# Kernel optimization log

Hardware: AMD Instinct MI355X
Metric: run time of the kernel (lower is better)

Reference implementation:

```python
import jax, jax.numpy as jnp
import numpy as np

EPS = 1e-6


def rms_norm(h, w):
    # T5-style: no mean subtraction, no bias; variance in fp32
    var = jnp.mean(jnp.square(h.astype(jnp.float32)), axis=-1, keepdims=True)
    h = h * jax.lax.rsqrt(var + EPS)
    return w * h


def split_heads(t, n_heads):
    b, n, d = t.shape
    return t.reshape(b, n, n_heads, d // n_heads).transpose(0, 2, 1, 3)  # [B,H,N,dk]


def unify_heads(t):
    b, h, n, dk = t.shape
    return t.transpose(0, 2, 1, 3).reshape(b, n, h * dk)


def attention(q_in, kv_in, bias, wq, wk, wv, wo, n_heads):
    q = split_heads(q_in @ wq, n_heads)   # [B,H,Nq,dk]
    k = split_heads(kv_in @ wk, n_heads)  # [B,H,Nk,dk]
    v = split_heads(kv_in @ wv, n_heads)
    scores = jnp.einsum('bhqd,bhkd->bhqk', q, k) + bias  # no 1/sqrt(dk) scaling (T5 style)
    w = jax.nn.softmax(scores.astype(jnp.float32), axis=-1).astype(scores.dtype)
    out = jnp.einsum('bhqk,bhkd->bhqd', w, v)
    return unify_heads(out) @ wo


def setup_inputs() -> dict:
    key = jax.random.key(0)
    ks = jax.random.split(key, 18)
    B, N, ENC_N, D, H, DFF = 4, 2048, 1024, 1024, 16, 4096
    s = 0.02
    inp = {
        'x': jax.random.normal(ks[0], (B, N, D), jnp.float32),
        'encoding': jax.random.normal(ks[1], (B, ENC_N, D), jnp.float32),
        'self_attention_position_bias': jax.random.normal(ks[2], (1, H, 1, N), jnp.float32),
        'enc_dec_attention_position_bias': jax.random.normal(ks[3], (1, H, N, ENC_N), jnp.float32),
        'wq_s': jax.random.normal(ks[4], (D, D), jnp.float32) * s,
        'wk_s': jax.random.normal(ks[5], (D, D), jnp.float32) * s,
        'wv_s': jax.random.normal(ks[6], (D, D), jnp.float32) * s,
        'wo_s': jax.random.normal(ks[7], (D, D), jnp.float32) * s,
        'wq_c': jax.random.normal(ks[8], (D, D), jnp.float32) * s,
        'wk_c': jax.random.normal(ks[9], (D, D), jnp.float32) * s,
        'wv_c': jax.random.normal(ks[10], (D, D), jnp.float32) * s,
        'wo_c': jax.random.normal(ks[11], (D, D), jnp.float32) * s,
        'ff1_w': jax.random.normal(ks[12], (D, DFF), jnp.float32) * s,
        'ff2_w': jax.random.normal(ks[13], (DFF, D), jnp.float32) * s,
        'norm1_w': jnp.ones((D,), jnp.float32),
        'norm2_w': jnp.ones((D,), jnp.float32),
        'norm3_w': jnp.ones((D,), jnp.float32),
    }
    return inp


def reference(x, encoding, self_attention_position_bias, enc_dec_attention_position_bias,
              wq_s, wk_s, wv_s, wo_s, wq_c, wk_c, wv_c, wo_c,
              ff1_w, ff2_w, norm1_w, norm2_w, norm3_w):
    n_heads = 16
    # --- self-attention (decoder: single query = last token) ---
    normed = rms_norm(x, norm1_w)
    q_in = normed[:, -1:, :]  # [B,1,D]
    attn_out = attention(q_in, normed, self_attention_position_bias,
                         wq_s, wk_s, wv_s, wo_s, n_heads)  # [B,1,D]
    x = x + attn_out  # broadcast over sequence, matching torch in-place broadcast
    # --- cross-attention ---
    normed = rms_norm(x, norm2_w)
    cross_out = attention(normed, encoding, enc_dec_attention_position_bias,
                          wq_c, wk_c, wv_c, wo_c, n_heads)  # [B,N,D]
    x = x + cross_out
    # --- MLP ---
    normed = rms_norm(x, norm3_w)
    mlp_out = jax.nn.relu(normed @ ff1_w) @ ff2_w
    return x + mlp_out
```

## Files before the change

kernel.cpp:

```cpp
#include <hip/hip_runtime.h>
#include <stdint.h>

typedef unsigned short bfu;
typedef __bf16 bf8v __attribute__((ext_vector_type(8)));
typedef unsigned short us8 __attribute__((ext_vector_type(8)));
typedef unsigned short us4 __attribute__((ext_vector_type(4)));
typedef float f4v __attribute__((ext_vector_type(4)));

__device__ __forceinline__ float bf2f(bfu u) {
    union { unsigned u; float f; } c; c.u = ((unsigned)u) << 16; return c.f;
}
__device__ __forceinline__ bfu f2bf(float f) {
    union { float f; unsigned u; } c; c.f = f;
    unsigned r = c.u + 0x7fffu + ((c.u >> 16) & 1u);
    return (bfu)(r >> 16);
}
__device__ __forceinline__ f4v mfma16(us8 a, us8 b, f4v c) {
    return __builtin_amdgcn_mfma_f32_16x16x32_bf16(
        __builtin_bit_cast(bf8v, a), __builtin_bit_cast(bf8v, b), c, 0, 0, 0);
}

template<int BM, int BN, int EPI>
__global__ __launch_bounds__(256) void gemm_bt(
    const bfu* __restrict__ A, const bfu* __restrict__ Bt,
    const float* __restrict__ resF, void* __restrict__ outP,
    int K, int lda, int ldb, int ldc)
{
    constexpr int BK = 64;
    constexpr int WM = BM / 2, WN = BN / 2;
    constexpr int TM = WM / 16, TN = WN / 16;
    __shared__ __align__(16) bfu sA[BM * BK];
    __shared__ __align__(16) bfu sB[BN * BK];

    const int tid  = threadIdx.x;
    const int lane = tid & 63;
    const int wid  = tid >> 6;
    const int wr = wid >> 1, wc = wid & 1;

    const int m0 = blockIdx.y * BM;
    const int n0 = blockIdx.x * BN;

    f4v acc[TM][TN];
    #pragma unroll
    for (int i = 0; i < TM; ++i)
        #pragma unroll
        for (int j = 0; j < TN; ++j)
            acc[i][j] = (f4v)0.0f;

    const bfu* gA = A + (long long)m0 * lda;
    const bfu* gB = Bt + (long long)n0 * ldb;
    const int rsub = tid >> 3;
    const int kb   = (tid & 7) * 8;

    for (int k0 = 0; k0 < K; k0 += BK) {
        us8 ra[BM / 32], rb[BN / 32];
        #pragma unroll
        for (int it = 0; it < BM / 32; ++it)
            ra[it] = *(const us8*)(gA + (long long)(it * 32 + rsub) * lda + k0 + kb);
        #pragma unroll
        for (int it = 0; it < BN / 32; ++it)
            rb[it] = *(const us8*)(gB + (long long)(it * 32 + rsub) * ldb + k0 + kb);

        __syncthreads();
        #pragma unroll
        for (int it = 0; it < BM / 32; ++it)
            *(us8*)&sA[(it * 32 + rsub) * BK + kb] = ra[it];
        #pragma unroll
        for (int it = 0; it < BN / 32; ++it)
            *(us8*)&sB[(it * 32 + rsub) * BK + kb] = rb[it];
        __syncthreads();

        #pragma unroll
        for (int kk = 0; kk < BK; kk += 32) {
            const int kro = kk + ((lane >> 4) << 3);
            us8 af[TM], bfr[TN];
            #pragma unroll
            for (int i = 0; i < TM; ++i)
                af[i] = *(const us8*)&sA[(wr * WM + i * 16 + (lane & 15)) * BK + kro];
            #pragma unroll
            for (int j = 0; j < TN; ++j)
                bfr[j] = *(const us8*)&sB[(wc * WN + j * 16 + (lane & 15)) * BK + kro];
            #pragma unroll
            for (int i = 0; i < TM; ++i)
                #pragma unroll
                for (int j = 0; j < TN; ++j)
                    acc[i][j] = mfma16(af[i], bfr[j], acc[i][j]);
        }
    }

    const int quad = lane >> 4;
    const int cn = lane & 15;
    #pragma unroll
    for (int i = 0; i < TM; ++i) {
        #pragma unroll
        for (int j = 0; j < TN; ++j) {
            const int col = n0 + wc * WN + j * 16 + cn;
            #pragma unroll
            for (int r = 0; r < 4; ++r) {
                const int row = m0 + wr * WM + i * 16 + quad * 4 + r;
                const long long idx = (long long)row * ldc + col;
                const float v = acc[i][j][r];
                if constexpr (EPI == 0) ((bfu*)outP)[idx] = f2bf(v);
                else if constexpr (EPI == 1) ((float*)outP)[idx] = resF[idx] + v;
                else ((bfu*)outP)[idx] = f2bf(fmaxf(v, 0.0f));
            }
        }
    }
}

#define SROW 1036
__global__ __launch_bounds__(256, 4) void xattn(
    const bfu* __restrict__ q2,
    const bfu* __restrict__ kv2,
    const bfu* __restrict__ v2t,
    const float* __restrict__ bias,
    bfu* __restrict__ O)
{
    __shared__ __align__(16) bfu S[16 * SROW];
    const int tid = threadIdx.x, lane = tid & 63, wid = tid >> 6;
    const int quad = lane >> 4, l16 = lane & 15;
    const int bh = blockIdx.x;
    const int b = bh >> 4, h = bh & 15;
    const int q0 = blockIdx.y * 16;

    const float* bp = bias + ((long long)h * 2048 + q0 + wid * 4) * 1024 + lane * 16;
    f4v br0[4], br1[4];
    #pragma unroll
    for (int j = 0; j < 4; ++j) br0[j] = *(const f4v*)(bp + j * 4);
    #pragma unroll
    for (int j = 0; j < 4; ++j) br1[j] = *(const f4v*)(bp + 1024 + j * 4);

    const int kh0 = wid * 256;
    const bfu* qbase = q2 + ((long long)b * 2048 + q0) * 1024 + h * 64;
    const us8 af0 = *(const us8*)(qbase + (long long)l16 * 1024 + quad * 8);
    const us8 af1 = *(const us8*)(qbase + (long long)l16 * 1024 + 32 + quad * 8);
    const bfu* kbase = kv2 + (long long)b * 2097152 + h * 64;
    #pragma unroll 4
    for (int t = 0; t < 16; ++t) {
        const int n0 = kh0 + t * 16;
        const bfu* kr = kbase + (long long)(n0 + l16) * 2048 + quad * 8;
        const us8 bf0 = *(const us8*)kr;
        const us8 bf1 = *(const us8*)(kr + 32);
        f4v acc = (f4v)0.0f;
        acc = mfma16(af0, bf0, acc);
        acc = mfma16(af1, bf1, acc);
        #pragma unroll
        for (int r = 0; r < 4; ++r)
            S[(quad * 4 + r) * SROW + n0 + l16] = f2bf(acc[r]);
    }
    f4v br2[4], br3[4];
    #pragma unroll
    for (int j = 0; j < 4; ++j) br2[j] = *(const f4v*)(bp + 2048 + j * 4);
    #pragma unroll
    for (int j = 0; j < 4; ++j) br3[j] = *(const f4v*)(bp + 3072 + j * 4);
    __syncthreads();

    auto dorow = [&](int row, const f4v bv[4]) {
        bfu* sp = &S[row * SROW + lane * 16];
        const us8 s0 = *(const us8*)sp;
        const us8 s1 = *(const us8*)(sp + 8);
        float v[16];
        #pragma unroll
        for (int j = 0; j < 8; ++j) v[j] = bf2f(s0[j]) + bv[j >> 2][j & 3];
        #pragma unroll
        for (int j = 0; j < 8; ++j) v[8 + j] = bf2f(s1[j]) + bv[2 + (j >> 2)][j & 3];
        float m = v[0];
        #pragma unroll
        for (int j = 1; j < 16; ++j) m = fmaxf(m, v[j]);
        #pragma unroll
        for (int o = 32; o; o >>= 1) m = fmaxf(m, __shfl_xor(m, o));
        float s = 0.f;
        #pragma unroll
        for (int j = 0; j < 16; ++j) { v[j] = __expf(v[j] - m); s += v[j]; }
        #pragma unroll
        for (int o = 32; o; o >>= 1) s += __shfl_xor(s, o);
        const float inv = 1.0f / s;
        us8 o0, o1;
        #pragma unroll
        for (int j = 0; j < 8; ++j) { o0[j] = f2bf(v[j] * inv); o1[j] = f2bf(v[8 + j] * inv); }
        *(us8*)sp = o0;
        *(us8*)(sp + 8) = o1;
    };
    dorow(wid * 4 + 0, br0);
    dorow(wid * 4 + 1, br1);
    dorow(wid * 4 + 2, br2);
    dorow(wid * 4 + 3, br3);
    __syncthreads();

    const bfu* vb = v2t + (long long)bh * 65536 + (long long)(wid * 16 + l16) * 1024;
    f4v a0 = (f4v)0.0f, a1 = (f4v)0.0f;
    for (int k0 = 0; k0 < 1024; k0 += 256) {
        us8 pa[8], vf[8];
        #pragma unroll
        for (int j = 0; j < 8; ++j) {
            pa[j] = *(const us8*)&S[l16 * SROW + k0 + j * 32 + quad * 8];
            vf[j] = *(const us8*)(vb + k0 + j * 32 + quad * 8);
        }
        #pragma unroll
        for (int j = 0; j < 8; j += 2) {
            a0 = mfma16(pa[j],     vf[j],     a0);
            a1 = mfma16(pa[j + 1], vf[j + 1], a1);
        }
    }
    const f4v acc3 = a0 + a1;
    bfu* ob = O + ((long long)b * 2048 + q0) * 1024 + h * 64 + wid * 16;
    #pragma unroll
    for (int r = 0; r < 4; ++r)
        ob[(long long)(quad * 4 + r) * 1024 + l16] = f2bf(acc3[r]);
}

__global__ __launch_bounds__(256) void cvt_f2b(
    const float* __restrict__ in, bfu* __restrict__ out)
{
    const long long i = ((long long)blockIdx.x * 256 + threadIdx.x) * 4;
    f4v v = *(const f4v*)(in + i);
    us4 o;
    #pragma unroll
    for (int k = 0; k < 4; ++k) o[k] = f2bf(v[k]);
    *(us4*)(out + i) = o;
}

__global__ __launch_bounds__(256) void transpose_plain(
    const float* __restrict__ in, bfu* __restrict__ out, int R, int C)
{
    __shared__ bfu t[32][33];
    const int r0 = blockIdx.y * 32, c0 = blockIdx.x * 32;
    const int tx = threadIdx.x, ty = threadIdx.y;
    #pragma unroll
    for (int i = 0; i < 32; i += 8)
        t[ty + i][tx] = f2bf(in[(long long)(r0 + ty + i) * C + c0 + tx]);
    __syncthreads();
    #pragma unroll
    for (int i = 0; i < 32; i += 8)
        out[(long long)(c0 + ty + i) * R + r0 + tx] = t[tx][ty + i];
}

__global__ __launch_bounds__(256) void transpose_w8(
    const float* p0, const float* p1, const float* p2, const float* p3,
    const float* p4, const float* p5, const float* p6, const float* p7,
    bfu* __restrict__ out)
{
    __shared__ bfu t[32][33];
    const float* srcs[8] = {p0, p1, p2, p3, p4, p5, p6, p7};
    const int zz = blockIdx.z;
    const float* in = srcs[zz];
    bfu* o = out + (long long)zz * 1048576;
    const int r0 = blockIdx.y * 32, c0 = blockIdx.x * 32;
    const int tx = threadIdx.x, ty = threadIdx.y;
    #pragma unroll
    for (int i = 0; i < 32; i += 8)
        t[ty + i][tx] = f2bf(in[(long long)(r0 + ty + i) * 1024 + c0 + tx]);
    __syncthreads();
    #pragma unroll
    for (int i = 0; i < 32; i += 8)
        o[(long long)(c0 + ty + i) * 1024 + r0 + tx] = t[tx][ty + i];
}

__global__ __launch_bounds__(256) void transpose_v2(
    const bfu* __restrict__ kv2, bfu* __restrict__ v2t)
{
    __shared__ bfu t[32][33];
    const int z = blockIdx.z, b = z >> 4, h = z & 15;
    const bfu* in = kv2 + (long long)b * 2097152 + 1024 + h * 64;
    bfu* o = v2t + (long long)z * 65536;
    const int c0 = blockIdx.x * 32, r0 = blockIdx.y * 32;
    const int tx = threadIdx.x, ty = threadIdx.y;
    #pragma unroll
    for (int i = 0; i < 32; i += 8)
        t[ty + i][tx] = in[(long long)(r0 + ty + i) * 2048 + c0 + tx];
    __syncthreads();
    #pragma unroll
    for (int i = 0; i < 32; i += 8)
        o[(long long)(c0 + ty + i) * 1024 + r0 + tx] = t[tx][ty + i];
}

__device__ __forceinline__ float blockSum4(float v, float* red) {
    const int lane = threadIdx.x & 63, wid = threadIdx.x >> 6;
    #pragma unroll
    for (int o = 32; o; o >>= 1) v += __shfl_xor(v, o);
    if (lane == 0) red[wid] = v;
    __syncthreads();
    return red[0] + red[1] + red[2] + red[3];
}

__global__ __launch_bounds__(256) void rmsnorm_f32k(
    const float* __restrict__ X, const float* __restrict__ w, bfu* __restrict__ O)
{
    __shared__ float red[4];
    const long long row = blockIdx.x;
    const int tid = threadIdx.x;
    f4v xv = *(const f4v*)(X + row * 1024 + tid * 4);
    float ss = 0.f;
    #pragma unroll
    for (int i = 0; i < 4; ++i) ss += xv[i] * xv[i];
    ss = blockSum4(ss, red);
    const float sc = rsqrtf(ss * (1.0f / 1024.0f) + 1e-6f);
    f4v wv = *(const f4v*)(w + tid * 4);
    us4 o4;
    #pragma unroll
    for (int i = 0; i < 4; ++i) o4[i] = f2bf(xv[i] * sc * wv[i]);
    *(us4*)(O + row * 1024 + tid * 4) = o4;
}

__global__ __launch_bounds__(256) void add_bcast_rmsnorm(
    const float* __restrict__ X, const float* __restrict__ attn,
    const float* __restrict__ w, float* __restrict__ X1, bfu* __restrict__ O)
{
    __shared__ float red[4];
    const long long row = blockIdx.x;
    const int b = (int)(row >> 11);
    const int tid = threadIdx.x;
    f4v xv = *(const f4v*)(X + row * 1024 + tid * 4);
    f4v av = *(const f4v*)(attn + b * 1024 + tid * 4);
    f4v v;
    float ss = 0.f;
    #pragma unroll
    for (int i = 0; i < 4; ++i) { v[i] = xv[i] + av[i]; ss += v[i] * v[i]; }
    *(f4v*)(X1 + row * 1024 + tid * 4) = v;
    ss = blockSum4(ss, red);
    const float sc = rsqrtf(ss * (1.0f / 1024.0f) + 1e-6f);
    f4v wv = *(const f4v*)(w + tid * 4);
    us4 o4;
    #pragma unroll
    for (int i = 0; i < 4; ++i) o4[i] = f2bf(v[i] * sc * wv[i]);
    *(us4*)(O + row * 1024 + tid * 4) = o4;
}

template<int OUTF>
__global__ __launch_bounds__(256) void vecmat(
    const bfu* __restrict__ A, const bfu* __restrict__ Bt, void* __restrict__ out,
    int K, int N, long long aStride, long long aBase)
{
    __shared__ float sa[1024];
    const int tid = threadIdx.x;
    const int b = blockIdx.y;
    const bfu* ar = A + aBase + (long long)b * aStride;
    for (int k = tid; k < K; k += 256) sa[k] = bf2f(ar[k]);
    __syncthreads();
    const int n = blockIdx.x * 256 + tid;
    if (n < N) {
        const bfu* wr = Bt + (long long)n * K;
        float s = 0.f;
        for (int k = 0; k < K; k += 8) {
            us8 wv = *(const us8*)(wr + k);
            #pragma unroll
            for (int j = 0; j < 8; ++j) s += sa[k + j] * bf2f(wv[j]);
        }
        if constexpr (OUTF) ((float*)out)[(long long)b * N + n] = s;
        else ((bfu*)out)[(long long)b * N + n] = f2bf(s);
    }
}

__global__ __launch_bounds__(256) void decode_attn(
    const bfu* __restrict__ qs, const bfu* __restrict__ KV,
    const float* __restrict__ bias, bfu* __restrict__ osmall)
{
    const int bh = blockIdx.x, b = bh >> 4, h = bh & 15;
    const int tid = threadIdx.x, lane = tid & 63, wid = tid >> 6;
    __shared__ float sq[64];
    __shared__ float sc[2048];
    __shared__ float red[4];
    __shared__ float po[4][64];
    if (tid < 64) sq[tid] = bf2f(qs[b * 1024 + h * 64 + tid]);
    __syncthreads();

    const bfu* Kb = KV + (long long)b * 2048 * 2048 + h * 64;
    float lmax = -1e30f;
    for (int k = tid; k < 2048; k += 256) {
        const us8* kr = (const us8*)(Kb + (long long)k * 2048);
        float s = 0.f;
        #pragma unroll
        for (int j = 0; j < 8; ++j) {
            us8 kv = kr[j];
            #pragma unroll
            for (int t = 0; t < 8; ++t) s += sq[j * 8 + t] * bf2f(kv[t]);
        }
        s += bias[h * 2048 + k];
        sc[k] = s;
        lmax = fmaxf(lmax, s);
    }
    #pragma unroll
    for (int o = 32; o; o >>= 1) lmax = fmaxf(lmax, __shfl_xor(lmax, o));
    if (lane == 0) red[wid] = lmax;
    __syncthreads();
    const float m = fmaxf(fmaxf(red[0], red[1]), fmaxf(red[2], red[3]));
    __syncthreads();

    float lsum = 0.f;
    for (int k = tid; k < 2048; k += 256) {
        const float e = __expf(sc[k] - m);
        sc[k] = e; lsum += e;
    }
    #pragma unroll
    for (int o = 32; o; o >>= 1) lsum += __shfl_xor(lsum, o);
    if (lane == 0) red[wid] = lsum;
    __syncthreads();
    const float S = red[0] + red[1] + red[2] + red[3];

    const bfu* Vb = KV + (long long)b * 2048 * 2048 + 1024 + h * 64;
    const int d = tid & 63, ks = tid >> 6;
    float a = 0.f;
    for (int k = ks * 512; k < ks * 512 + 512; ++k)
        a += sc[k] * bf2f(Vb[(long long)k * 2048 + d]);
    po[ks][d] = a;
    __syncthreads();
    if (tid < 64) {
        const float r = (po[0][tid] + po[1][tid] + po[2][tid] + po[3][tid]) / S;
        osmall[b * 1024 + h * 64 + tid] = f2bf(r);
    }
}

extern "C" void kernel_launch(void* const* d_in, const int* in_sizes, int n_in,
                              void* d_out, int out_size, void* d_ws, size_t ws_size,
                              hipStream_t stream) {
    (void)in_sizes; (void)n_in; (void)out_size; (void)ws_size;
    const float* x     = (const float*)d_in[0];
    const float* enc   = (const float*)d_in[1];
    const float* sbias = (const float*)d_in[2];
    const float* cbias = (const float*)d_in[3];
    const float* wq_s  = (const float*)d_in[4];
    const float* wk_s  = (const float*)d_in[5];
    const float* wv_s  = (const float*)d_in[6];
    const float* wo_s  = (const float*)d_in[7];
    const float* wq_c  = (const float*)d_in[8];
    const float* wk_c  = (const float*)d_in[9];
    const float* wv_c  = (const float*)d_in[10];
    const float* wo_c  = (const float*)d_in[11];
    const float* ff1   = (const float*)d_in[12];
    const float* ff2   = (const float*)d_in[13];
    const float* n1w   = (const float*)d_in[14];
    const float* n2w   = (const float*)d_in[15];
    const float* n3w   = (const float*)d_in[16];
    float* out = (float*)d_out;

    char* ws = (char*)d_ws;
    size_t off = 0;
    auto alloc = [&](size_t bytes) -> void* {
        void* p = (void*)(ws + off);
        off += (bytes + 255) & ~(size_t)255;
        return p;
    };
    bfu*   normed = (bfu*)alloc((size_t)8192 * 1024 * 2);
    bfu*   kvs    = (bfu*)alloc((size_t)8192 * 2048 * 2);
    bfu*   obuf   = (bfu*)alloc((size_t)8192 * 1024 * 2);
    bfu*   v2t    = (bfu*)alloc((size_t)4096 * 1024 * 2);
    bfu*   encb   = (bfu*)alloc((size_t)4096 * 1024 * 2);
    float* x1f    = (float*)alloc((size_t)8192 * 1024 * 4);
    bfu*   wT     = (bfu*)alloc((size_t)8 * 1048576 * 2);
    bfu*   ff1T   = (bfu*)alloc((size_t)4096 * 1024 * 2);
    bfu*   ff2T   = (bfu*)alloc((size_t)4096 * 1024 * 2);
    bfu*   qsb    = (bfu*)alloc(4 * 1024 * 2);
    bfu*   osm    = (bfu*)alloc(4 * 1024 * 2);
    float* attnv  = (float*)alloc(4 * 1024 * 4);
    bfu*   q2b = kvs;
    bfu*   kv2 = kvs + (size_t)8192 * 1024;
    bfu*   H1  = kvs;

    const dim3 tb32(32, 8);

    cvt_f2b<<<dim3(4096), 256, 0, stream>>>(enc, encb);
    transpose_w8<<<dim3(32, 32, 8), tb32, 0, stream>>>(
        wq_s, wk_s, wv_s, wo_s, wq_c, wk_c, wv_c, wo_c, wT);
    transpose_plain<<<dim3(128, 32, 1), tb32, 0, stream>>>(ff1, ff1T, 1024, 4096);
    transpose_plain<<<dim3(32, 128, 1), tb32, 0, stream>>>(ff2, ff2T, 4096, 1024);

    rmsnorm_f32k<<<dim3(8192), 256, 0, stream>>>(x, n1w, normed);

    gemm_bt<128, 128, 0><<<dim3(16, 64), 256, 0, stream>>>(
        normed, wT + 1 * 1048576, nullptr, kvs, 1024, 1024, 1024, 2048);
    vecmat<0><<<dim3(4, 4), 256, 0, stream>>>(normed, wT + 0 * 1048576, qsb,
        1024, 1024, (long long)2048 * 1024, (long long)2047 * 1024);
    decode_attn<<<dim3(64), 256, 0, stream>>>(qsb, kvs, sbias, osm);
    vecmat<1><<<dim3(4, 4), 256, 0, stream>>>(osm, wT + 3 * 1048576, attnv,
        1024, 1024, 1024, 0);
    add_bcast_rmsnorm<<<dim3(8192), 256, 0, stream>>>(x, attnv, n2w, x1f, normed);

    gemm_bt<128, 64, 0><<<dim3(16, 64), 256, 0, stream>>>(
        normed, wT + 4 * 1048576, nullptr, q2b, 1024, 1024, 1024, 1024);
    gemm_bt<128, 64, 0><<<dim3(32, 32), 256, 0, stream>>>(
        encb, wT + 5 * 1048576, nullptr, kv2, 1024, 1024, 1024, 2048);
    transpose_v2<<<dim3(2, 32, 64), tb32, 0, stream>>>(kv2, v2t);

    xattn<<<dim3(64, 128), 256, 0, stream>>>(q2b, kv2, v2t, cbias, obuf);

    gemm_bt<128, 64, 1><<<dim3(16, 64), 256, 0, stream>>>(
        obuf, wT + 7 * 1048576, x1f, x1f, 1024, 1024, 1024, 1024);

    rmsnorm_f32k<<<dim3(8192), 256, 0, stream>>>(x1f, n3w, normed);
    gemm_bt<128, 128, 2><<<dim3(32, 64), 256, 0, stream>>>(
        normed, ff1T, nullptr, H1, 1024, 1024, 1024, 4096);
    gemm_bt<128, 64, 1><<<dim3(16, 64), 256, 0, stream>>>(
        H1, ff2T, x1f, out, 4096, 4096, 4096, 1024);
}
```

Measured before the change: 1.106 ms.

## Rewrite cross-attention as register-resident flash attention with 32x32 MFMA

Replaces the LDS-staged score/softmax/PV cross-attention kernel with an online-softmax loop where each wave owns 32 query rows and streams K, V and bias in 32-key tiles. Scores stay in registers and are converted to bf16 via packed cvt and lane shuffles to form the PV MFMA operand, using 32x32x16 MFMAs. Rescaling of the output accumulators is skipped unless the running max grows by more than a threshold. The grid shrinks from 8192 to 1024 blocks with no shared memory, trading parallelism and per-block latency hiding for less LDS traffic and fewer syncs.

```diff
diff --git a/kernel.cpp b/kernel.cpp
--- a/kernel.cpp
+++ b/kernel.cpp
@@ -6,6 +6,7 @@
 typedef unsigned short us8 __attribute__((ext_vector_type(8)));
 typedef unsigned short us4 __attribute__((ext_vector_type(4)));
 typedef float f4v __attribute__((ext_vector_type(4)));
+typedef float f16v __attribute__((ext_vector_type(16)));
 
 __device__ __forceinline__ float bf2f(bfu u) {
     union { unsigned u; float f; } c; c.u = ((unsigned)u) << 16; return c.f;
@@ -18,6 +19,20 @@
 __device__ __forceinline__ f4v mfma16(us8 a, us8 b, f4v c) {
     return __builtin_amdgcn_mfma_f32_16x16x32_bf16(
         __builtin_bit_cast(bf8v, a), __builtin_bit_cast(bf8v, b), c, 0, 0, 0);
+}
+__device__ __forceinline__ f16v mfma32(us8 a, us8 b, f16v c) {
+    return __builtin_amdgcn_mfma_f32_32x32x16_bf16(
+        __builtin_bit_cast(bf8v, a), __builtin_bit_cast(bf8v, b), c, 0, 0, 0);
+}
+__device__ __forceinline__ unsigned cvtpk(float lo, float hi) {
+    unsigned r;
+    asm("v_cvt_pk_bf16_f32 %0, %1, %2" : "=v"(r) : "v"(lo), "v"(hi));
+    return r;
+}
+__device__ __forceinline__ us8 mkfrag(unsigned w0, unsigned w1, unsigned w2, unsigned w3) {
+    union { unsigned w[4]; us8 v; } u;
+    u.w[0] = w0; u.w[1] = w1; u.w[2] = w2; u.w[3] = w3;
+    return u.v;
 }
 
 template<int BM, int BN, int EPI>
@@ -108,105 +123,112 @@
     }
 }
 
-#define SROW 1036
-__global__ __launch_bounds__(256, 4) void xattn(
+__global__ __launch_bounds__(256) void xattn(
     const bfu* __restrict__ q2,
     const bfu* __restrict__ kv2,
     const bfu* __restrict__ v2t,
     const float* __restrict__ bias,
     bfu* __restrict__ O)
 {
-    __shared__ __align__(16) bfu S[16 * SROW];
     const int tid = threadIdx.x, lane = tid & 63, wid = tid >> 6;
-    const int quad = lane >> 4, l16 = lane & 15;
-    const int bh = blockIdx.x;
-    const int b = bh >> 4, h = bh & 15;
-    const int q0 = blockIdx.y * 16;
-
-    const float* bp = bias + ((long long)h * 2048 + q0 + wid * 4) * 1024 + lane * 16;
-    f4v br0[4], br1[4];
-    #pragma unroll
-    for (int j = 0; j < 4; ++j) br0[j] = *(const f4v*)(bp + j * 4);
-    #pragma unroll
-    for (int j = 0; j < 4; ++j) br1[j] = *(const f4v*)(bp + 1024 + j * 4);
-
-    const int kh0 = wid * 256;
-    const bfu* qbase = q2 + ((long long)b * 2048 + q0) * 1024 + h * 64;
-    const us8 af0 = *(const us8*)(qbase + (long long)l16 * 1024 + quad * 8);
-    const us8 af1 = *(const us8*)(qbase + (long long)l16 * 1024 + 32 + quad * 8);
-    const bfu* kbase = kv2 + (long long)b * 2097152 + h * 64;
-    #pragma unroll 4
-    for (int t = 0; t < 16; ++t) {
-        const int n0 = kh0 + t * 16;
-        const bfu* kr = kbase + (long long)(n0 + l16) * 2048 + quad * 8;
-        const us8 bf0 = *(const us8*)kr;
-        const us8 bf1 = *(const us8*)(kr + 32);
-        f4v acc = (f4v)0.0f;
-        acc = mfma16(af0, bf0, acc);
-        acc = mfma16(af1, bf1, acc);
-        #pragma unroll
-        for (int r = 0; r < 4; ++r)
-            S[(quad * 4 + r) * SROW + n0 + l16] = f2bf(acc[r]);
-    }
-    f4v br2[4], br3[4];
-    #pragma unroll
-    for (int j = 0; j < 4; ++j) br2[j] = *(const f4v*)(bp + 2048 + j * 4);
-    #pragma unroll
-    for (int j = 0; j < 4; ++j) br3[j] = *(const f4v*)(bp + 3072 + j * 4);
-    __syncthreads();
-
-    auto dorow = [&](int row, const f4v bv[4]) {
-        bfu* sp = &S[row * SROW + lane * 16];
-        const us8 s0 = *(const us8*)sp;
-        const us8 s1 = *(const us8*)(sp + 8);
-        float v[16];
-        #pragma unroll
-        for (int j = 0; j < 8; ++j) v[j] = bf2f(s0[j]) + bv[j >> 2][j & 3];
-        #pragma unroll
-        for (int j = 0; j < 8; ++j) v[8 + j] = bf2f(s1[j]) + bv[2 + (j >> 2)][j & 3];
-        float m = v[0];
-        #pragma unroll
-        for (int j = 1; j < 16; ++j) m = fmaxf(m, v[j]);
-        #pragma unroll
-        for (int o = 32; o; o >>= 1) m = fmaxf(m, __shfl_xor(m, o));
-        float s = 0.f;
-        #pragma unroll
-        for (int j = 0; j < 16; ++j) { v[j] = __expf(v[j] - m); s += v[j]; }
-        #pragma unroll
-        for (int o = 32; o; o >>= 1) s += __shfl_xor(s, o);
-        const float inv = 1.0f / s;
-        us8 o0, o1;
-        #pragma unroll
-        for (int j = 0; j < 8; ++j) { o0[j] = f2bf(v[j] * inv); o1[j] = f2bf(v[8 + j] * inv); }
-        *(us8*)sp = o0;
-        *(us8*)(sp + 8) = o1;
-    };
-    dorow(wid * 4 + 0, br0);
-    dorow(wid * 4 + 1, br1);
-    dorow(wid * 4 + 2, br2);
-    dorow(wid * 4 + 3, br3);
-    __syncthreads();
-
-    const bfu* vb = v2t + (long long)bh * 65536 + (long long)(wid * 16 + l16) * 1024;
-    f4v a0 = (f4v)0.0f, a1 = (f4v)0.0f;
-    for (int k0 = 0; k0 < 1024; k0 += 256) {
-        us8 pa[8], vf[8];
-        #pragma unroll
-        for (int j = 0; j < 8; ++j) {
-            pa[j] = *(const us8*)&S[l16 * SROW + k0 + j * 32 + quad * 8];
-            vf[j] = *(const us8*)(vb + k0 + j * 32 + quad * 8);
+    const int l32 = lane & 31, hi = lane >> 5;
+    const int bh = blockIdx.x, b = bh >> 4, h = bh & 15;
+    const int q0 = blockIdx.y * 128 + wid * 32;
+
+    const bfu* qrow = q2 + (long long)(b * 2048 + q0 + l32) * 1024 + h * 64 + hi * 8;
+    const us8 qf0 = *(const us8*)(qrow);
+    const us8 qf1 = *(const us8*)(qrow + 16);
+    const us8 qf2 = *(const us8*)(qrow + 32);
+    const us8 qf3 = *(const us8*)(qrow + 48);
+
+    const bfu* krow  = kv2 + (long long)b * 2097152 + (long long)l32 * 2048 + h * 64 + hi * 8;
+    const bfu* vrow0 = v2t + (long long)bh * 65536 + (long long)l32 * 1024 + hi * 8;
+    const bfu* vrow1 = vrow0 + 32 * 1024;
+    const float* brow = bias + (long long)(h * 2048 + q0 + l32) * 1024 + hi * 4;
+
+    f16v o0 = (f16v)0.0f, o1 = (f16v)0.0f;
+    float mrun = -3.0e38f, lrun = 0.0f;
+
+    for (int kt = 0; kt < 32; ++kt) {
+        const bfu* kp = krow + (long long)kt * 65536;
+        const us8 kf0 = *(const us8*)(kp);
+        const us8 kf1 = *(const us8*)(kp + 16);
+        const us8 kf2 = *(const us8*)(kp + 32);
+        const us8 kf3 = *(const us8*)(kp + 48);
+        f16v p = (f16v)0.0f;
+        p = mfma32(kf0, qf0, p);
+        p = mfma32(kf1, qf1, p);
+        p = mfma32(kf2, qf2, p);
+        p = mfma32(kf3, qf3, p);
+
+        const float* bp = brow + kt * 32;
+        const f4v b0 = *(const f4v*)(bp);
+        const f4v b1 = *(const f4v*)(bp + 8);
+        const f4v b2 = *(const f4v*)(bp + 16);
+        const f4v b3 = *(const f4v*)(bp + 24);
+        p[0] += b0[0];  p[1] += b0[1];  p[2] += b0[2];  p[3] += b0[3];
+        p[4] += b1[0];  p[5] += b1[1];  p[6] += b1[2];  p[7] += b1[3];
+        p[8] += b2[0];  p[9] += b2[1];  p[10] += b2[2]; p[11] += b2[3];
+        p[12] += b3[0]; p[13] += b3[1]; p[14] += b3[2]; p[15] += b3[3];
+
+        const float ma = fmaxf(fmaxf(p[0], p[1]), fmaxf(p[2], p[3]));
+        const float mb = fmaxf(fmaxf(p[4], p[5]), fmaxf(p[6], p[7]));
+        const float mc = fmaxf(fmaxf(p[8], p[9]), fmaxf(p[10], p[11]));
+        const float md = fmaxf(fmaxf(p[12], p[13]), fmaxf(p[14], p[15]));
+        float tmax = fmaxf(fmaxf(ma, mb), fmaxf(mc, md));
+        tmax = fmaxf(tmax, __shfl_xor(tmax, 32));
+
+        if (!__all(tmax <= mrun + 8.0f)) {
+            const float mnew = fmaxf(mrun, tmax);
+            const float alpha = __expf(mrun - mnew);
+            lrun *= alpha;
+            #pragma unroll
+            for (int r = 0; r < 16; ++r) {
+                const float ar = __shfl(alpha, (r & 3) + 8 * (r >> 2) + 4 * hi);
+                o0[r] *= ar; o1[r] *= ar;
+            }
+            mrun = mnew;
         }
-        #pragma unroll
-        for (int j = 0; j < 8; j += 2) {
-            a0 = mfma16(pa[j],     vf[j],     a0);
-            a1 = mfma16(pa[j + 1], vf[j + 1], a1);
-        }
-    }
-    const f4v acc3 = a0 + a1;
-    bfu* ob = O + ((long long)b * 2048 + q0) * 1024 + h * 64 + wid * 16;
-    #pragma unroll
-    for (int r = 0; r < 4; ++r)
-        ob[(long long)(quad * 4 + r) * 1024 + l16] = f2bf(acc3[r]);
+
+        #pragma unroll
+        for (int r = 0; r < 16; ++r) p[r] = __expf(p[r] - mrun);
+
+        const float sa = (p[0] + p[1]) + (p[2] + p[3]);
+        const float sb = (p[4] + p[5]) + (p[6] + p[7]);
+        const float sc = (p[8] + p[9]) + (p[10] + p[11]);
+        const float sd = (p[12] + p[13]) + (p[14] + p[15]);
+        float tsum = (sa + sb) + (sc + sd);
+        tsum += __shfl_xor(tsum, 32);
+        lrun += tsum;
+
+        const unsigned A0 = cvtpk(p[0], p[1]),   A1 = cvtpk(p[2], p[3]);
+        const unsigned B0 = cvtpk(p[4], p[5]),   B1 = cvtpk(p[6], p[7]);
+        const unsigned C0 = cvtpk(p[8], p[9]),   C1 = cvtpk(p[10], p[11]);
+        const unsigned D0 = cvtpk(p[12], p[13]), D1 = cvtpk(p[14], p[15]);
+        const unsigned s0 = (unsigned)__shfl_xor((int)(hi ? A0 : B0), 32);
+        const unsigned s1 = (unsigned)__shfl_xor((int)(hi ? A1 : B1), 32);
+        const unsigned s2 = (unsigned)__shfl_xor((int)(hi ? C0 : D0), 32);
+        const unsigned s3 = (unsigned)__shfl_xor((int)(hi ? C1 : D1), 32);
+        const us8 F0 = mkfrag(hi ? s0 : A0, hi ? s1 : A1, hi ? B0 : s0, hi ? B1 : s1);
+        const us8 F1 = mkfrag(hi ? s2 : C0, hi ? s3 : C1, hi ? D0 : s2, hi ? D1 : s3);
+
+        const bfu* vp0 = vrow0 + kt * 32;
+        const bfu* vp1 = vrow1 + kt * 32;
+        o0 = mfma32(F0, *(const us8*)(vp0), o0);
+        o0 = mfma32(F1, *(const us8*)(vp0 + 16), o0);
+        o1 = mfma32(F0, *(const us8*)(vp1), o1);
+        o1 = mfma32(F1, *(const us8*)(vp1 + 16), o1);
+    }
+
+    const float linv = 1.0f / lrun;
+    bfu* ob = O + (long long)(b * 2048 + q0) * 1024 + h * 64 + l32;
+    #pragma unroll
+    for (int r = 0; r < 16; ++r) {
+        const int qr = (r & 3) + 8 * (r >> 2) + 4 * hi;
+        const float li = __shfl(linv, qr);
+        ob[(long long)qr * 1024]      = f2bf(o0[r] * li);
+        ob[(long long)qr * 1024 + 32] = f2bf(o1[r] * li);
+    }
 }
 
 __global__ __launch_bounds__(256) void cvt_f2b(
@@ -481,7 +503,7 @@
         encb, wT + 5 * 1048576, nullptr, kv2, 1024, 1024, 1024, 2048);
     transpose_v2<<<dim3(2, 32, 64), tb32, 0, stream>>>(kv2, v2t);
 
-    xattn<<<dim3(64, 128), 256, 0, stream>>>(q2b, kv2, v2t, cbias, obuf);
+    xattn<<<dim3(64, 16), 256, 0, stream>>>(q2b, kv2, v2t, cbias, obuf);
 
     gemm_bt<128, 64, 1><<<dim3(16, 64), 256, 0, stream>>>(
         obuf, wT + 7 * 1048576, x1f, x1f, 1024, 1024, 1024, 1024);
```

Result: faster. 1.040 ms (-6.0%).
